# Performance work log

Measured on AMD Instinct MI355X. Metric: run time of the kernel, lower is better.

## Reference

```python
import jax, jax.numpy as jnp
import numpy as np

B, S, T = 256, 512, 20
VOCAB, E, H, SKIP = 100000, 25, 128, 64


def _lstm_scan(x, skip, mask, K, R, Sk, b):
    # x:[S,B,E], skip:[S,B,SKIP], mask:[S,B] bool. Keras RNN mask semantics:
    # masked steps carry previous h/c and emit previous h.
    Bn = x.shape[1]
    Hn = R.shape[0]
    def step(carry, inp):
        h, c = carry
        xt, st, mt = inp
        z = xt @ K + h @ R + st @ Sk + b            # [B,4H]
        zi, zf, zg, zo = jnp.split(z, 4, axis=-1)
        cn = jax.nn.sigmoid(zf) * c + jax.nn.sigmoid(zi) * jnp.tanh(zg)
        hn = jax.nn.sigmoid(zo) * jnp.tanh(cn)
        m = mt[:, None]
        h2 = jnp.where(m, hn, h)
        c2 = jnp.where(m, cn, c)
        return (h2, c2), h2
    init = (jnp.zeros((Bn, Hn), x.dtype), jnp.zeros((Bn, Hn), x.dtype))
    (hF, cF), hs = jax.lax.scan(step, init, (x, skip, mask))
    return hs, hF


def setup_inputs() -> dict:
    key = jax.random.key(0)
    ks = jax.random.split(key, 20)
    p = lambda k, shp: jax.random.normal(k, shp, dtype=jnp.float32) * 0.05
    inp = {
        "input_tags": jax.random.randint(ks[0], (B, S, T), 0, VOCAB, dtype=jnp.int32),
        "embedded_skips": jax.random.normal(ks[1], (B, S, SKIP), dtype=jnp.float32),
        "emb_table": p(ks[2], (VOCAB, E)),
        "kernel_f": p(ks[3], (E, 4 * H)),
        "rec_f": p(ks[4], (H, 4 * H)),
        "skip_f": p(ks[5], (SKIP, 4 * H)),
        "bias_f": jnp.zeros((4 * H,), jnp.float32),
        "kernel_b": p(ks[6], (E, 4 * H)),
        "rec_b": p(ks[7], (H, 4 * H)),
        "skip_b": p(ks[8], (SKIP, 4 * H)),
        "bias_b": jnp.zeros((4 * H,), jnp.float32),
        "Wk": p(ks[9], (2 * H, H)),
        "bk": jnp.zeros((H,), jnp.float32),
        "Wq": p(ks[10], (H, H)),
        "bq": jnp.zeros((H,), jnp.float32),
        "We": p(ks[11], (H, 1)),
        "be": jnp.zeros((1,), jnp.float32),
    }
    return inp


def reference(input_tags, embedded_skips, emb_table,
              kernel_f, rec_f, skip_f, bias_f,
              kernel_b, rec_b, skip_b, bias_b,
              Wk, bk, Wq, bq, We, be):
    mask3 = input_tags != 0                          # [B,S,T]
    emb = emb_table[input_tags]                      # [B,S,T,E]
    num_mask = mask3.astype(emb.dtype)
    summed = jnp.sum(emb * num_mask[..., None], axis=2)   # [B,S,E]
    denom = jnp.sum(num_mask, axis=2)                     # [B,S]
    denom = jnp.where(denom == 0, jnp.ones_like(denom), denom)
    gru_inp = summed / denom[..., None]                   # [B,S,E]
    step_mask = mask3[:, :, 0]                            # [B,S]

    # time-major for scan
    x_t = jnp.swapaxes(gru_inp, 0, 1)
    s_t = jnp.swapaxes(embedded_skips, 0, 1)
    m_t = jnp.swapaxes(step_mask, 0, 1)

    hs_f, h_fwd = _lstm_scan(x_t, s_t, m_t, kernel_f, rec_f, skip_f, bias_f)
    hs_b_rev, _ = _lstm_scan(x_t[::-1], s_t[::-1], m_t[::-1], kernel_b, rec_b, skip_b, bias_b)
    hs_b = hs_b_rev[::-1]
    out = jnp.swapaxes(jnp.concatenate([hs_f, hs_b], axis=-1), 0, 1)  # [B,S,2H]

    keys = out @ Wk + bk                                  # [B,S,H]
    queries = (h_fwd @ Wq + bq)[:, None, :]               # [B,1,H]
    energy = jnp.tanh(keys + queries) @ We + be           # [B,S,1]
    energy = energy + (1.0 - step_mask.astype(energy.dtype))[..., None] * -1e9
    weights = jax.nn.softmax(energy, axis=1)
    context = jnp.sum(weights * out, axis=1)              # [B,2H]
    return context
```

## Files before the change

kernel.cpp:

```cpp
#include <hip/hip_runtime.h>
#include <math.h>

#define Bb 256
#define Ss 512
#define Tt 20
#define Ee 25
#define Hh 128
#define SKIPn 64
#define H4n 512
#define BSn (Bb*Ss)
#define MG 4
#define HP 160
#define ZP 520
#define AP 264
#define LOG2E 1.4426950408889634f

typedef _Float16 f16x8 __attribute__((ext_vector_type(8)));
typedef _Float16 f16x4 __attribute__((ext_vector_type(4)));
typedef float f32x4 __attribute__((ext_vector_type(4)));

__device__ __forceinline__ float rcpf(float x) { return __builtin_amdgcn_rcpf(x); }
__device__ __forceinline__ float exp2f_(float x) { return __builtin_amdgcn_exp2f(x); }

__device__ __forceinline__ void lgkm_barrier() {
    __asm__ __volatile__("" ::: "memory");
    __builtin_amdgcn_s_waitcnt(0xC07F);
    __builtin_amdgcn_s_barrier();
    __asm__ __volatile__("" ::: "memory");
}

#define POOL_BLOCKS (BSn / 8)
#define CVT_BLOCKS  (BSn * SKIPn / (256 * 8))
__global__ void __launch_bounds__(256)
prep_kernel(const int* __restrict__ tags, const float* __restrict__ table,
            const float* __restrict__ skips,
            _Float16* __restrict__ gru16, float* __restrict__ maskf,
            float* __restrict__ maskt, _Float16* __restrict__ sk16) {
    if (blockIdx.x >= POOL_BLOCKS) {
        size_t i = ((size_t)(blockIdx.x - POOL_BLOCKS) * 256 + threadIdx.x) * 8;
        f32x4 a = *(const f32x4*)(skips + i);
        f32x4 b = *(const f32x4*)(skips + i + 4);
        f16x8 o;
#pragma unroll
        for (int j = 0; j < 4; j++) { o[j] = (_Float16)a[j]; o[j + 4] = (_Float16)b[j]; }
        *(f16x8*)(sk16 + i) = o;
        return;
    }
    int group = blockIdx.x * 8 + (threadIdx.x >> 5);
    int lane = threadIdx.x & 31;
    int b = group >> 9;
    int t = group & (Ss - 1);
    const int* tg = tags + (size_t)group * Tt;
    const int el = (lane < Ee) ? lane : (Ee - 1);

    int tagv[Tt];
#pragma unroll
    for (int tt = 0; tt < Tt; tt++) tagv[tt] = tg[tt];

    float vv[Tt];
#pragma unroll
    for (int tt = 0; tt < Tt; tt++)
        vv[tt] = table[(size_t)tagv[tt] * Ee + el];

    float acc = 0.0f;
    int cnt = 0;
#pragma unroll
    for (int tt = 0; tt < Tt; tt++) {
        const bool nz = (tagv[tt] != 0);
        cnt += nz ? 1 : 0;
        acc += nz ? vv[tt] : 0.0f;
    }
    float scale = rcpf((float)(cnt > 0 ? cnt : 1));
    float v = (lane < Ee) ? acc * scale : 0.0f;
    gru16[((size_t)t * Bb + b) * 32 + lane] = (_Float16)v;
    if (lane == 0) {
        float m = (tagv[0] != 0) ? 1.0f : 0.0f;
        maskf[group] = m;
        maskt[(size_t)t * Bb + b] = m;
    }
}

__global__ void __launch_bounds__(512)
__attribute__((amdgpu_waves_per_eu(2, 2)))
scan_kernel(const _Float16* __restrict__ gru16, const _Float16* __restrict__ sk16,
            const float* __restrict__ maskt,
            const float* __restrict__ Kf, const float* __restrict__ Rf,
            const float* __restrict__ Skf, const float* __restrict__ bf,
            const float* __restrict__ Kb, const float* __restrict__ Rb,
            const float* __restrict__ Skb, const float* __restrict__ bb,
            _Float16* __restrict__ hs16, float* __restrict__ hfwd)
{
    __shared__ __align__(16) _Float16 h16[2 * MG * HP];
    __shared__ __align__(16) _Float16 zlds[2][16 * 4 * ZP];

    const int tid = threadIdx.x;
    const int lane = tid & 63;
    const int w = tid >> 6;
    const int l16 = lane & 15;
    const int q = lane >> 4;
    const int mb = l16 >> 2;
    const int bg = blockIdx.x & 63;
    const int dir = blockIdx.x >> 6;
    const int b0 = bg * MG;
    const int col = 16 * w + l16;

    const float* Kw = dir ? Kb : Kf;
    const float* Rw = dir ? Rb : Rf;
    const float* Sw = dir ? Skb : Skf;
    const float* bw = dir ? bb : bf;
    const float gs[4] = {LOG2E, LOG2E, 2.0f * LOG2E, LOG2E};

    f16x8 hfr[4][4];
#pragma unroll
    for (int kt = 0; kt < 4; kt++) {
#pragma unroll
        for (int g = 0; g < 4; g++) {
            const int n = g * Hh + col;
            f16x8 v;
#pragma unroll
            for (int j = 0; j < 8; j++)
                v[j] = (_Float16)(Rw[(32 * kt + 8 * q + j) * H4n + n] * gs[g]);
            hfr[kt][g] = v;
        }
    }
    f16x8 bx[4], bs0[4], bs1[4];
    f32x4 biasA[4];
#pragma unroll
    for (int g = 0; g < 4; g++) {
        const int n = g * Hh + col;
        f16x8 vx, v0, v1;
#pragma unroll
        for (int j = 0; j < 8; j++) {
            const int kk = 8 * q + j;
            vx[j] = (_Float16)(((kk < Ee) ? Kw[kk * H4n + n] : 0.0f) * gs[g]);
            v0[j] = (_Float16)(Sw[kk * H4n + n] * gs[g]);
            v1[j] = (_Float16)(Sw[(32 + kk) * H4n + n] * gs[g]);
        }
        bx[g] = vx; bs0[g] = v0; bs1[g] = v1;
        const float bv = bw[g * Hh + col] * gs[g];
        f32x4 ba = {bv, bv, bv, bv};
        biasA[g] = ba;
    }
    const f32x4 zacc4 = {0.0f, 0.0f, 0.0f, 0.0f};

    for (int idx = tid; idx < 2 * MG * HP; idx += 512) h16[idx] = (_Float16)0.0f;

    float c = 0.0f, h = 0.0f;

    const int tsub = l16 >> 2, bbn = l16 & 3;
    const int tg0 = dir ? (Ss - 1 - tsub) : tsub;
    const _Float16* px = gru16 + ((size_t)tg0 * Bb + b0 + bbn) * 32 + 8 * q;
    const _Float16* ps = sk16 + ((size_t)(b0 + bbn) * Ss + tg0) * SKIPn + 8 * q;
    ptrdiff_t pxd = (dir ? -4 : 4) * (ptrdiff_t)(Bb * 32);
    ptrdiff_t psd = (dir ? -4 : 4) * (ptrdiff_t)SKIPn;

    const float* mpf = maskt + (size_t)(dir ? (Ss - 1) : 0) * Bb + b0 + q;
    const ptrdiff_t mdelta = dir ? -(ptrdiff_t)Bb : (ptrdiff_t)Bb;
    float mreg[2];
    mreg[0] = mpf[0]; mreg[1] = mpf[mdelta];
    mpf += 2 * mdelta;

    _Float16* hsp = hs16 + ((size_t)(b0 + q) * Ss + (dir ? Ss - 1 : 0)) * (2 * Hh)
                    + dir * Hh + col;
    const ptrdiff_t odelta = dir ? -(2 * Hh) : (2 * Hh);

    f16x8 gx, g0, g1;
    auto ldA = [&]() {
        gx = *(const f16x8*)px;
        g0 = *(const f16x8*)ps;
        g1 = *(const f16x8*)(ps + 32);
        px += pxd; ps += psd;
    };

    f32x4 zc[4];

    ldA();
#pragma unroll
    for (int T = 0; T < 4; T++) {
        const f16x8 ax = gx, a0 = g0, a1 = g1;
        ldA();
#pragma unroll
        for (int g = 0; g < 4; g++) {
            zc[g] = __builtin_amdgcn_mfma_f32_16x16x32_f16(ax, bx[g],  biasA[g], 0, 0, 0);
            zc[g] = __builtin_amdgcn_mfma_f32_16x16x32_f16(a0, bs0[g], zc[g], 0, 0, 0);
            zc[g] = __builtin_amdgcn_mfma_f32_16x16x32_f16(a1, bs1[g], zc[g], 0, 0, 0);
        }
        _Float16* zw = &zlds[0][0] + ((4 * T + q) * 4) * ZP + col * 4;
#pragma unroll
        for (int r = 0; r < 4; r++) {
            f16x4 o;
            o[0] = (_Float16)zc[0][r]; o[1] = (_Float16)zc[1][r];
            o[2] = (_Float16)zc[2][r]; o[3] = (_Float16)zc[3][r];
            *(f16x4*)(zw + r * ZP) = o;
        }
    }
    __syncthreads();

#pragma unroll 1
    for (int k = 0; k < 32; ++k) {
        const _Float16* zr = &zlds[k & 1][0];
        _Float16* zwb = &zlds[(k + 1) & 1][0];

#pragma unroll
        for (int j = 0; j < 16; ++j) {
            const int T = j >> 2, ph = j & 3;

            const _Float16* hb = h16 + (j & 1) * (MG * HP);
            const f16x8 ah0 = *(const f16x8*)(hb + mb * HP +  0 + 8 * q);
            const f16x8 ah1 = *(const f16x8*)(hb + mb * HP + 32 + 8 * q);
            const f16x8 ah2 = *(const f16x8*)(hb + mb * HP + 64 + 8 * q);
            const f16x8 ah3 = *(const f16x8*)(hb + mb * HP + 96 + 8 * q);
            const f16x4 z4 = *(const f16x4*)(zr + (j * 4 + q) * ZP + col * 4);

            f32x4 accA[4], accB[4];
#pragma unroll
            for (int g = 0; g < 4; g++) {
                accA[g] = __builtin_amdgcn_mfma_f32_16x16x32_f16(ah0, hfr[0][g], zacc4, 0, 0, 0);
                accB[g] = __builtin_amdgcn_mfma_f32_16x16x32_f16(ah1, hfr[1][g], zacc4, 0, 0, 0);
                accA[g] = __builtin_amdgcn_mfma_f32_16x16x32_f16(ah2, hfr[2][g], accA[g], 0, 0, 0);
                accB[g] = __builtin_amdgcn_mfma_f32_16x16x32_f16(ah3, hfr[3][g], accB[g], 0, 0, 0);
            }

            if (ph == 0) {
#pragma unroll
                for (int g = 0; g < 4; g++)
                    zc[g] = __builtin_amdgcn_mfma_f32_16x16x32_f16(gx, bx[g], biasA[g], 0, 0, 0);
            } else if (ph == 1) {
#pragma unroll
                for (int g = 0; g < 4; g++)
                    zc[g] = __builtin_amdgcn_mfma_f32_16x16x32_f16(g0, bs0[g], zc[g], 0, 0, 0);
            } else if (ph == 2) {
#pragma unroll
                for (int g = 0; g < 4; g++)
                    zc[g] = __builtin_amdgcn_mfma_f32_16x16x32_f16(g1, bs1[g], zc[g], 0, 0, 0);
                if (j == 10 && k == 30) { pxd = 0; psd = 0; }
                ldA();
            } else {
                _Float16* zw = zwb + ((4 * T + q) * 4) * ZP + col * 4;
#pragma unroll
                for (int r = 0; r < 4; r++) {
                    f16x4 o;
                    o[0] = (_Float16)zc[0][r]; o[1] = (_Float16)zc[1][r];
                    o[2] = (_Float16)zc[2][r]; o[3] = (_Float16)zc[3][r];
                    *(f16x4*)(zw + r * ZP) = o;
                }
            }

            const float mk = mreg[j & 1];
            mreg[j & 1] = *mpf; mpf += mdelta;
            const float zi = accA[0][0] + accB[0][0] + (float)z4[0];
            const float zf = accA[1][0] + accB[1][0] + (float)z4[1];
            const float zg = accA[2][0] + accB[2][0] + (float)z4[2];
            const float zo = accA[3][0] + accB[3][0] + (float)z4[3];
            const float ei = exp2f_(-zi);
            const float ef = exp2f_(-zf);
            const float eg = exp2f_(-zg);
            const float eo = exp2f_(-zo);
            const float pi = 1.0f + ei, pg = 1.0f + eg, pf = 1.0f + ef;
            const float p  = pi * pg;
            const float t1 = (1.0f - eg) * pf;
            const float cn = fmaf(c, p, t1) * rcpf(pf * p);
            const float ec = exp2f_(cn * (-2.0f * LOG2E));
            const float hn = (1.0f - ec) * rcpf((1.0f + eo) * (1.0f + ec));
            const bool mm = (mk != 0.0f);
            c = mm ? cn : c;
            h = mm ? hn : h;

            _Float16* hw = h16 + ((j + 1) & 1) * (MG * HP);
            hw[q * HP + col] = (_Float16)h;
            *hsp = (_Float16)h;
            hsp += odelta;
            lgkm_barrier();
        }
    }

    if (dir == 0) hfwd[(size_t)(b0 + q) * Hh + col] = h;
}

__global__ void __launch_bounds__(512)
attn_kernel(const _Float16* __restrict__ hs16, const float* __restrict__ hfwd,
            const float* __restrict__ Wq, const float* __restrict__ bq,
            const float* __restrict__ bk,
            const float* __restrict__ Wk, const float* __restrict__ We,
            const float* __restrict__ maskf, float* __restrict__ outp)
{
    __shared__ float hfl[Hh];
    __shared__ float qpart[4][Hh];
    __shared__ float qtot_s[Hh];
    __shared__ float epart[8][16];
    __shared__ float psh[16];
    __shared__ float mls[Ss];
    __shared__ float dls[16];
    __shared__ float ctxp[16][2 * Hh + 1];
    __shared__ __align__(16) _Float16 atile[2][16 * AP];

    const int tid = threadIdx.x;
    const int lane = tid & 63;
    const int w = tid >> 6;
    const int l16 = lane & 15;
    const int q = lane >> 4;
    const int b = blockIdx.x;
    const int j = 16 * w + l16;
    const int seg = tid >> 5;
    const int cg = tid & 31;

    f16x8 bk16[8];
#pragma unroll
    for (int kt = 0; kt < 8; kt++) {
        f16x8 v;
#pragma unroll
        for (int jj = 0; jj < 8; jj++)
            v[jj] = (_Float16)Wk[(32 * kt + 8 * q + jj) * Hh + j];
        bk16[kt] = v;
    }
    const float wej = We[j];

    mls[tid] = maskf[(size_t)b * Ss + tid];
    if (tid < Hh) hfl[tid] = hfwd[(size_t)b * Hh + tid];
    __syncthreads();
    {
        const int jj = tid & 127, sg = tid >> 7;
        float p = 0.0f;
#pragma unroll
        for (int k = 0; k < 32; k++)
            p += hfl[32 * sg + k] * Wq[(32 * sg + k) * Hh + jj];
        qpart[sg][jj] = p;
    }
    __syncthreads();
    if (tid < Hh)
        qtot_s[tid] = qpart[0][tid] + qpart[1][tid] + qpart[2][tid] + qpart[3][tid]
                      + bq[tid] + bk[tid];
    __syncthreads();
    const float qj = qtot_s[j];

    const _Float16* hb = hs16 + (size_t)b * Ss * (2 * Hh);
    *(f16x8*)(&atile[0][seg * AP + cg * 8]) =
        *(const f16x8*)(hb + (size_t)seg * (2 * Hh) + cg * 8);
    float ctxa[8];
#pragma unroll
    for (int jj = 0; jj < 8; jj++) ctxa[jj] = 0.0f;
    float dsum = 0.0f;
    __syncthreads();

#pragma unroll 1
    for (int st = 0; st < 32; st++) {
        const int p = st & 1;
        f16x8 sreg;
        if (st < 31)
            sreg = *(const f16x8*)(hb + (size_t)((st + 1) * 16 + seg) * (2 * Hh) + cg * 8);

        f32x4 acc0 = {0.f, 0.f, 0.f, 0.f}, acc1 = {0.f, 0.f, 0.f, 0.f};
#pragma unroll
        for (int kt = 0; kt < 4; kt++) {
            const f16x8 a = *(const f16x8*)(&atile[p][l16 * AP + kt * 32 + 8 * q]);
            acc0 = __builtin_amdgcn_mfma_f32_16x16x32_f16(a, bk16[kt], acc0, 0, 0, 0);
        }
#pragma unroll
        for (int kt = 4; kt < 8; kt++) {
            const f16x8 a = *(const f16x8*)(&atile[p][l16 * AP + kt * 32 + 8 * q]);
            acc1 = __builtin_amdgcn_mfma_f32_16x16x32_f16(a, bk16[kt], acc1, 0, 0, 0);
        }
        float vals[4];
#pragma unroll
        for (int r = 0; r < 4; r++) {
            const float x = acc0[r] + acc1[r] + qj;
            const float e = exp2f_(fminf(x * (-2.0f * LOG2E), 80.0f));
            vals[r] = (1.0f - e) * rcpf(1.0f + e) * wej;
        }
#pragma unroll
        for (int m = 1; m < 16; m <<= 1) {
#pragma unroll
            for (int r = 0; r < 4; r++) vals[r] += __shfl_xor(vals[r], m);
        }
        if (l16 == 0) {
#pragma unroll
            for (int r = 0; r < 4; r++) epart[w][4 * q + r] = vals[r];
        }
        __syncthreads();
        if (tid < 16) {
            float e = epart[0][tid] + epart[1][tid] + epart[2][tid] + epart[3][tid]
                    + epart[4][tid] + epart[5][tid] + epart[6][tid] + epart[7][tid];
            psh[tid] = mls[st * 16 + tid] * exp2f_(e * LOG2E);
        }
        __syncthreads();
        {
            const float wv = psh[seg];
            const f16x8 hv = *(const f16x8*)(&atile[p][seg * AP + cg * 8]);
#pragma unroll
            for (int jj = 0; jj < 8; jj++) ctxa[jj] = fmaf(wv, (float)hv[jj], ctxa[jj]);
            dsum += wv;
        }
        if (st < 31)
            *(f16x8*)(&atile[p ^ 1][seg * AP + cg * 8]) = sreg;
        __syncthreads();
    }

#pragma unroll
    for (int jj = 0; jj < 8; jj++) ctxp[seg][8 * cg + jj] = ctxa[jj];
    if (cg == 0) dls[seg] = dsum;
    __syncthreads();
    if (tid < 2 * Hh) {
        float s = 0.0f;
#pragma unroll
        for (int sg = 0; sg < 16; sg++) s += ctxp[sg][tid];
        float d = 0.0f;
#pragma unroll
        for (int sg = 0; sg < 16; sg++) d += dls[sg];
        outp[(size_t)b * (2 * Hh) + tid] = s * rcpf(d);
    }
}

extern "C" void kernel_launch(void* const* d_in, const int* in_sizes, int n_in,
                              void* d_out, int out_size, void* d_ws, size_t ws_size,
                              hipStream_t stream) {
    const int*   tags  = (const int*)d_in[0];
    const float* skips = (const float*)d_in[1];
    const float* table = (const float*)d_in[2];
    const float* Kf    = (const float*)d_in[3];
    const float* Rf    = (const float*)d_in[4];
    const float* Skf   = (const float*)d_in[5];
    const float* bf    = (const float*)d_in[6];
    const float* Kb    = (const float*)d_in[7];
    const float* Rb    = (const float*)d_in[8];
    const float* Skb   = (const float*)d_in[9];
    const float* bb    = (const float*)d_in[10];
    const float* Wk    = (const float*)d_in[11];
    const float* bk    = (const float*)d_in[12];
    const float* Wq    = (const float*)d_in[13];
    const float* bq    = (const float*)d_in[14];
    const float* We    = (const float*)d_in[15];

    char* ws = (char*)d_ws;
    _Float16* gru16 = (_Float16*)ws; ws += (size_t)BSn * 32 * 2;
    _Float16* sk16  = (_Float16*)ws; ws += (size_t)BSn * SKIPn * 2;
    float* maskf = (float*)ws; ws += (size_t)BSn * 4;
    float* maskt_base = (float*)ws; ws += ((size_t)BSn + 4 * Bb) * 4;
    float* maskt = maskt_base + 2 * Bb;
    _Float16* hs16 = (_Float16*)ws; ws += (size_t)BSn * 2 * Hh * 2;
    float* hfwd  = (float*)ws; ws += (size_t)Bb * Hh * 4;

    prep_kernel<<<POOL_BLOCKS + CVT_BLOCKS, 256, 0, stream>>>(
        tags, table, skips, gru16, maskf, maskt, sk16);
    scan_kernel<<<128, 512, 0, stream>>>(gru16, sk16, maskt,
                                         Kf, Rf, Skf, bf,
                                         Kb, Rb, Skb, bb,
                                         hs16, hfwd);
    attn_kernel<<<Bb, 512, 0, stream>>>(hs16, hfwd, Wq, bq, bk, Wk, We, maskf,
                                        (float*)d_out);
}
```

Before: 466.5 us.

## Split LSTM scan into 256 blocks of 2 batch rows with 4 waves

The recurrent scan now runs 256 workgroups of 256 threads, each handling 2 batch rows instead of 4, with each wave covering 32 hidden columns through two MFMA column groups. The input projection is spread over 8 phases per step, and the z staging buffer is re-laid out. The goal is to use more CUs and cut the per-step barrier cost on the serial critical path. In exchange, each wave issues twice as many recurrent MFMAs per step, and half of each 16-row MFMA tile is wasted on duplicate batch rows.

Measured after the change: 539.5 us. 15.6% more time.

```diff
diff --git a/kernel.cpp b/kernel.cpp
--- a/kernel.cpp
+++ b/kernel.cpp
@@ -9,9 +9,9 @@
 #define SKIPn 64
 #define H4n 512
 #define BSn (Bb*Ss)
-#define MG 4
+#define MG2 2
 #define HP 160
-#define ZP 520
+#define ZPR 516
 #define AP 264
 #define LOG2E 1.4426950408889634f
 
@@ -80,8 +80,8 @@
     }
 }
 
-__global__ void __launch_bounds__(512)
-__attribute__((amdgpu_waves_per_eu(2, 2)))
+__global__ void __launch_bounds__(256)
+__attribute__((amdgpu_waves_per_eu(1, 1)))
 scan_kernel(const _Float16* __restrict__ gru16, const _Float16* __restrict__ sk16,
             const float* __restrict__ maskt,
             const float* __restrict__ Kf, const float* __restrict__ Rf,
@@ -90,19 +90,21 @@
             const float* __restrict__ Skb, const float* __restrict__ bb,
             _Float16* __restrict__ hs16, float* __restrict__ hfwd)
 {
-    __shared__ __align__(16) _Float16 h16[2 * MG * HP];
-    __shared__ __align__(16) _Float16 zlds[2][16 * 4 * ZP];
+    __shared__ __align__(16) _Float16 h16[2 * MG2 * HP];
+    __shared__ __align__(16) _Float16 zlds[2][32 * ZPR];
 
     const int tid = threadIdx.x;
     const int lane = tid & 63;
     const int w = tid >> 6;
     const int l16 = lane & 15;
     const int q = lane >> 4;
-    const int mb = l16 >> 2;
-    const int bg = blockIdx.x & 63;
-    const int dir = blockIdx.x >> 6;
-    const int b0 = bg * MG;
-    const int col = 16 * w + l16;
+    const int qb = q >> 1;
+    const int cgq = q & 1;
+    const int col = 32 * w + cgq * 16 + l16;
+    const int ab = l16 >> 3;
+    const int bg = blockIdx.x & 127;
+    const int dir = blockIdx.x >> 7;
+    const int b0 = bg * MG2;
 
     const float* Kw = dir ? Kb : Kf;
     const float* Rw = dir ? Rb : Rf;
@@ -110,57 +112,63 @@
     const float* bw = dir ? bb : bf;
     const float gs[4] = {LOG2E, LOG2E, 2.0f * LOG2E, LOG2E};
 
-    f16x8 hfr[4][4];
+    f16x8 hfr[4][4][2];
 #pragma unroll
     for (int kt = 0; kt < 4; kt++) {
 #pragma unroll
         for (int g = 0; g < 4; g++) {
-            const int n = g * Hh + col;
-            f16x8 v;
-#pragma unroll
-            for (int j = 0; j < 8; j++)
-                v[j] = (_Float16)(Rw[(32 * kt + 8 * q + j) * H4n + n] * gs[g]);
-            hfr[kt][g] = v;
-        }
-    }
-    f16x8 bx[4], bs0[4], bs1[4];
-    f32x4 biasA[4];
+#pragma unroll
+            for (int cg = 0; cg < 2; cg++) {
+                const int n = g * Hh + 32 * w + cg * 16 + l16;
+                f16x8 v;
+#pragma unroll
+                for (int j = 0; j < 8; j++)
+                    v[j] = (_Float16)(Rw[(32 * kt + 8 * q + j) * H4n + n] * gs[g]);
+                hfr[kt][g][cg] = v;
+            }
+        }
+    }
+    f16x8 bx[4][2], bs0[4][2], bs1[4][2];
+    f32x4 biasA[4][2];
 #pragma unroll
     for (int g = 0; g < 4; g++) {
-        const int n = g * Hh + col;
-        f16x8 vx, v0, v1;
-#pragma unroll
-        for (int j = 0; j < 8; j++) {
-            const int kk = 8 * q + j;
-            vx[j] = (_Float16)(((kk < Ee) ? Kw[kk * H4n + n] : 0.0f) * gs[g]);
-            v0[j] = (_Float16)(Sw[kk * H4n + n] * gs[g]);
-            v1[j] = (_Float16)(Sw[(32 + kk) * H4n + n] * gs[g]);
-        }
-        bx[g] = vx; bs0[g] = v0; bs1[g] = v1;
-        const float bv = bw[g * Hh + col] * gs[g];
-        f32x4 ba = {bv, bv, bv, bv};
-        biasA[g] = ba;
+#pragma unroll
+        for (int cg = 0; cg < 2; cg++) {
+            const int n = g * Hh + 32 * w + cg * 16 + l16;
+            f16x8 vx, v0, v1;
+#pragma unroll
+            for (int j = 0; j < 8; j++) {
+                const int kk = 8 * q + j;
+                vx[j] = (_Float16)(((kk < Ee) ? Kw[kk * H4n + n] : 0.0f) * gs[g]);
+                v0[j] = (_Float16)(Sw[kk * H4n + n] * gs[g]);
+                v1[j] = (_Float16)(Sw[(32 + kk) * H4n + n] * gs[g]);
+            }
+            bx[g][cg] = vx; bs0[g][cg] = v0; bs1[g][cg] = v1;
+            const float bv = bw[g * Hh + n % Hh] * gs[g];
+            f32x4 ba = {bv, bv, bv, bv};
+            biasA[g][cg] = ba;
+        }
     }
     const f32x4 zacc4 = {0.0f, 0.0f, 0.0f, 0.0f};
 
-    for (int idx = tid; idx < 2 * MG * HP; idx += 512) h16[idx] = (_Float16)0.0f;
+    for (int idx = tid; idx < 2 * MG2 * HP; idx += 256) h16[idx] = (_Float16)0.0f;
 
     float c = 0.0f, h = 0.0f;
 
-    const int tsub = l16 >> 2, bbn = l16 & 3;
+    const int tsub = l16 >> 1, bbn = l16 & 1;
     const int tg0 = dir ? (Ss - 1 - tsub) : tsub;
     const _Float16* px = gru16 + ((size_t)tg0 * Bb + b0 + bbn) * 32 + 8 * q;
     const _Float16* ps = sk16 + ((size_t)(b0 + bbn) * Ss + tg0) * SKIPn + 8 * q;
-    ptrdiff_t pxd = (dir ? -4 : 4) * (ptrdiff_t)(Bb * 32);
-    ptrdiff_t psd = (dir ? -4 : 4) * (ptrdiff_t)SKIPn;
-
-    const float* mpf = maskt + (size_t)(dir ? (Ss - 1) : 0) * Bb + b0 + q;
+    ptrdiff_t pxd = (dir ? -8 : 8) * (ptrdiff_t)(Bb * 32);
+    ptrdiff_t psd = (dir ? -8 : 8) * (ptrdiff_t)SKIPn;
+
+    const float* mpf = maskt + (size_t)(dir ? (Ss - 1) : 0) * Bb + b0 + qb;
     const ptrdiff_t mdelta = dir ? -(ptrdiff_t)Bb : (ptrdiff_t)Bb;
     float mreg[2];
     mreg[0] = mpf[0]; mreg[1] = mpf[mdelta];
     mpf += 2 * mdelta;
 
-    _Float16* hsp = hs16 + ((size_t)(b0 + q) * Ss + (dir ? Ss - 1 : 0)) * (2 * Hh)
+    _Float16* hsp = hs16 + ((size_t)(b0 + qb) * Ss + (dir ? Ss - 1 : 0)) * (2 * Hh)
                     + dir * Hh + col;
     const ptrdiff_t odelta = dir ? -(2 * Hh) : (2 * Hh);
 
@@ -172,27 +180,34 @@
         px += pxd; ps += psd;
     };
 
-    f32x4 zc[4];
+    f32x4 zc[4][2];
+
+    auto zstore = [&](_Float16* zb, int T, int cg) {
+        _Float16* zw = zb + (T * 16 + 4 * q) * ZPR + (32 * w + cg * 16 + l16) * 4;
+#pragma unroll
+        for (int r = 0; r < 4; r++) {
+            f16x4 o;
+            o[0] = (_Float16)zc[0][cg][r]; o[1] = (_Float16)zc[1][cg][r];
+            o[2] = (_Float16)zc[2][cg][r]; o[3] = (_Float16)zc[3][cg][r];
+            *(f16x4*)(zw + r * ZPR) = o;
+        }
+    };
 
     ldA();
 #pragma unroll
-    for (int T = 0; T < 4; T++) {
+    for (int T = 0; T < 2; T++) {
         const f16x8 ax = gx, a0 = g0, a1 = g1;
         ldA();
 #pragma unroll
-        for (int g = 0; g < 4; g++) {
-            zc[g] = __builtin_amdgcn_mfma_f32_16x16x32_f16(ax, bx[g],  biasA[g], 0, 0, 0);
-            zc[g] = __builtin_amdgcn_mfma_f32_16x16x32_f16(a0, bs0[g], zc[g], 0, 0, 0);
-            zc[g] = __builtin_amdgcn_mfma_f32_16x16x32_f16(a1, bs1[g], zc[g], 0, 0, 0);
-        }
-        _Float16* zw = &zlds[0][0] + ((4 * T + q) * 4) * ZP + col * 4;
-#pragma unroll
-        for (int r = 0; r < 4; r++) {
-            f16x4 o;
-            o[0] = (_Float16)zc[0][r]; o[1] = (_Float16)zc[1][r];
-            o[2] = (_Float16)zc[2][r]; o[3] = (_Float16)zc[3][r];
-            *(f16x4*)(zw + r * ZP) = o;
-        }
+        for (int g = 0; g < 4; g++)
+#pragma unroll
+            for (int cg = 0; cg < 2; cg++) {
+                zc[g][cg] = __builtin_amdgcn_mfma_f32_16x16x32_f16(ax, bx[g][cg],  biasA[g][cg], 0, 0, 0);
+                zc[g][cg] = __builtin_amdgcn_mfma_f32_16x16x32_f16(a0, bs0[g][cg], zc[g][cg], 0, 0, 0);
+                zc[g][cg] = __builtin_amdgcn_mfma_f32_16x16x32_f16(a1, bs1[g][cg], zc[g][cg], 0, 0, 0);
+            }
+        zstore(&zlds[0][0], T, 0);
+        zstore(&zlds[0][0], T, 1);
     }
     __syncthreads();
 
@@ -203,55 +218,76 @@
 
 #pragma unroll
         for (int j = 0; j < 16; ++j) {
-            const int T = j >> 2, ph = j & 3;
-
-            const _Float16* hb = h16 + (j & 1) * (MG * HP);
-            const f16x8 ah0 = *(const f16x8*)(hb + mb * HP +  0 + 8 * q);
-            const f16x8 ah1 = *(const f16x8*)(hb + mb * HP + 32 + 8 * q);
-            const f16x8 ah2 = *(const f16x8*)(hb + mb * HP + 64 + 8 * q);
-            const f16x8 ah3 = *(const f16x8*)(hb + mb * HP + 96 + 8 * q);
-            const f16x4 z4 = *(const f16x4*)(zr + (j * 4 + q) * ZP + col * 4);
-
-            f32x4 accA[4], accB[4];
-#pragma unroll
-            for (int g = 0; g < 4; g++) {
-                accA[g] = __builtin_amdgcn_mfma_f32_16x16x32_f16(ah0, hfr[0][g], zacc4, 0, 0, 0);
-                accB[g] = __builtin_amdgcn_mfma_f32_16x16x32_f16(ah1, hfr[1][g], zacc4, 0, 0, 0);
-                accA[g] = __builtin_amdgcn_mfma_f32_16x16x32_f16(ah2, hfr[2][g], accA[g], 0, 0, 0);
-                accB[g] = __builtin_amdgcn_mfma_f32_16x16x32_f16(ah3, hfr[3][g], accB[g], 0, 0, 0);
-            }
+            const int T = j >> 3, ph = j & 7;
+
+            const _Float16* hb = h16 + (j & 1) * (MG2 * HP);
+            const f16x8 ah0 = *(const f16x8*)(hb + ab * HP +  0 + 8 * q);
+            const f16x8 ah1 = *(const f16x8*)(hb + ab * HP + 32 + 8 * q);
+            const f16x8 ah2 = *(const f16x8*)(hb + ab * HP + 64 + 8 * q);
+            const f16x8 ah3 = *(const f16x8*)(hb + ab * HP + 96 + 8 * q);
+            const f16x4 z4 = *(const f16x4*)(zr + ((j >> 3) * 16 + 2 * (j & 7) + qb) * ZPR + col * 4);
+
+            f32x4 acc[4][2];
+#pragma unroll
+            for (int g = 0; g < 4; g++)
+#pragma unroll
+                for (int cg = 0; cg < 2; cg++) {
+                    acc[g][cg] = __builtin_amdgcn_mfma_f32_16x16x32_f16(ah0, hfr[0][g][cg], zacc4, 0, 0, 0);
+                    acc[g][cg] = __builtin_amdgcn_mfma_f32_16x16x32_f16(ah1, hfr[1][g][cg], acc[g][cg], 0, 0, 0);
+                    acc[g][cg] = __builtin_amdgcn_mfma_f32_16x16x32_f16(ah2, hfr[2][g][cg], acc[g][cg], 0, 0, 0);
+                    acc[g][cg] = __builtin_amdgcn_mfma_f32_16x16x32_f16(ah3, hfr[3][g][cg], acc[g][cg], 0, 0, 0);
+                }
 
             if (ph == 0) {
 #pragma unroll
-                for (int g = 0; g < 4; g++)
-                    zc[g] = __builtin_amdgcn_mfma_f32_16x16x32_f16(gx, bx[g], biasA[g], 0, 0, 0);
+                for (int g = 0; g < 2; g++)
+#pragma unroll
+                    for (int cg = 0; cg < 2; cg++)
+                        zc[g][cg] = __builtin_amdgcn_mfma_f32_16x16x32_f16(gx, bx[g][cg], biasA[g][cg], 0, 0, 0);
             } else if (ph == 1) {
 #pragma unroll
-                for (int g = 0; g < 4; g++)
-                    zc[g] = __builtin_amdgcn_mfma_f32_16x16x32_f16(g0, bs0[g], zc[g], 0, 0, 0);
+                for (int g = 2; g < 4; g++)
+#pragma unroll
+                    for (int cg = 0; cg < 2; cg++)
+                        zc[g][cg] = __builtin_amdgcn_mfma_f32_16x16x32_f16(gx, bx[g][cg], biasA[g][cg], 0, 0, 0);
             } else if (ph == 2) {
 #pragma unroll
-                for (int g = 0; g < 4; g++)
-                    zc[g] = __builtin_amdgcn_mfma_f32_16x16x32_f16(g1, bs1[g], zc[g], 0, 0, 0);
-                if (j == 10 && k == 30) { pxd = 0; psd = 0; }
+                for (int g = 0; g < 2; g++)
+#pragma unroll
+                    for (int cg = 0; cg < 2; cg++)
+                        zc[g][cg] = __builtin_amdgcn_mfma_f32_16x16x32_f16(g0, bs0[g][cg], zc[g][cg], 0, 0, 0);
+            } else if (ph == 3) {
+#pragma unroll
+                for (int g = 2; g < 4; g++)
+#pragma unroll
+                    for (int cg = 0; cg < 2; cg++)
+                        zc[g][cg] = __builtin_amdgcn_mfma_f32_16x16x32_f16(g0, bs0[g][cg], zc[g][cg], 0, 0, 0);
+            } else if (ph == 4) {
+#pragma unroll
+                for (int g = 0; g < 2; g++)
+#pragma unroll
+                    for (int cg = 0; cg < 2; cg++)
+                        zc[g][cg] = __builtin_amdgcn_mfma_f32_16x16x32_f16(g1, bs1[g][cg], zc[g][cg], 0, 0, 0);
+            } else if (ph == 5) {
+#pragma unroll
+                for (int g = 2; g < 4; g++)
+#pragma unroll
+                    for (int cg = 0; cg < 2; cg++)
+                        zc[g][cg] = __builtin_amdgcn_mfma_f32_16x16x32_f16(g1, bs1[g][cg], zc[g][cg], 0, 0, 0);
+                if (k == 30 && j == 5) { pxd = 0; psd = 0; }
                 ldA();
+            } else if (ph == 6) {
+                zstore(zwb, T, 0);
             } else {
-                _Float16* zw = zwb + ((4 * T + q) * 4) * ZP + col * 4;
-#pragma unroll
-                for (int r = 0; r < 4; r++) {
-                    f16x4 o;
-                    o[0] = (_Float16)zc[0][r]; o[1] = (_Float16)zc[1][r];
-                    o[2] = (_Float16)zc[2][r]; o[3] = (_Float16)zc[3][r];
-                    *(f16x4*)(zw + r * ZP) = o;
-                }
+                zstore(zwb, T, 1);
             }
 
             const float mk = mreg[j & 1];
             mreg[j & 1] = *mpf; mpf += mdelta;
-            const float zi = accA[0][0] + accB[0][0] + (float)z4[0];
-            const float zf = accA[1][0] + accB[1][0] + (float)z4[1];
-            const float zg = accA[2][0] + accB[2][0] + (float)z4[2];
-            const float zo = accA[3][0] + accB[3][0] + (float)z4[3];
+            const float zi = (cgq ? acc[0][1][0] : acc[0][0][0]) + (float)z4[0];
+            const float zf = (cgq ? acc[1][1][0] : acc[1][0][0]) + (float)z4[1];
+            const float zg = (cgq ? acc[2][1][0] : acc[2][0][0]) + (float)z4[2];
+            const float zo = (cgq ? acc[3][1][0] : acc[3][0][0]) + (float)z4[3];
             const float ei = exp2f_(-zi);
             const float ef = exp2f_(-zf);
             const float eg = exp2f_(-zg);
@@ -266,15 +302,15 @@
             c = mm ? cn : c;
             h = mm ? hn : h;
 
-            _Float16* hw = h16 + ((j + 1) & 1) * (MG * HP);
-            hw[q * HP + col] = (_Float16)h;
+            _Float16* hw = h16 + ((j + 1) & 1) * (MG2 * HP);
+            hw[qb * HP + col] = (_Float16)h;
             *hsp = (_Float16)h;
             hsp += odelta;
             lgkm_barrier();
         }
     }
 
-    if (dir == 0) hfwd[(size_t)(b0 + q) * Hh + col] = h;
+    if (dir == 0) hfwd[(size_t)(b0 + qb) * Hh + col] = h;
 }
 
 __global__ void __launch_bounds__(512)
@@ -441,7 +477,7 @@
 
     prep_kernel<<<POOL_BLOCKS + CVT_BLOCKS, 256, 0, stream>>>(
         tags, table, skips, gru16, maskf, maskt, sk16);
-    scan_kernel<<<128, 512, 0, stream>>>(gru16, sk16, maskt,
+    scan_kernel<<<256, 256, 0, stream>>>(gru16, sk16, maskt,
                                          Kf, Rf, Skf, bf,
                                          Kb, Rb, Skb, bb,
                                          hs16, hfwd);
```
